# Kernel tuning notes

Hardware: AMD Instinct MI355X
Metric: run time of the kernel (lower is better)

Reference implementation:

```python
import jax, jax.numpy as jnp
import numpy as np

B, BAG, H, C = 512, 32, 1024, 53
EPS = 1e-8  # torch F.cosine_similarity denominator clamp


def setup_inputs() -> dict:
    key = jax.random.key(0)
    ks = jax.random.split(key, 5)
    return {
        "sent_reps": jax.random.normal(ks[0], (B, BAG, H), jnp.float32),
        "aug_sent_reps": jax.random.normal(ks[1], (B, BAG, H), jnp.float32),
        "rel_table": jax.random.normal(ks[2], (C, H), jnp.float32),
        "cls_w": jax.random.normal(ks[3], (C, H), jnp.float32) * 0.02,
        "cls_b": jnp.zeros((C,), jnp.float32),
        "labels": jax.random.randint(ks[4], (B,), 0, C),
        "temperature": jnp.asarray(0.1, jnp.float32),
    }


def _cl(rep, aug, bag_rep, T):
    # rep, aug: (B, bag, H); bag_rep: (B, H)
    nr = jnp.linalg.norm(rep, axis=-1)        # (B, bag)
    na = jnp.linalg.norm(aug, axis=-1)        # (B, bag)
    nb = jnp.linalg.norm(bag_rep, axis=-1)    # (B,)
    pos_sim = jnp.sum(rep * aug, axis=-1) / jnp.maximum(nr * na, EPS)  # (B, bag)
    pos = jnp.exp(pos_sim / T)
    # pair[c, j, b] = cos(rep[b, j], bag_rep[c])  -- matches torch permute/broadcast chain
    dots = jnp.einsum('bjh,ch->cjb', rep, bag_rep)               # (B, bag, B)
    denom = jnp.maximum(nb[:, None, None] * nr.T[None], EPS)      # (B, bag, B)
    pair = dots / denom
    idx = jnp.arange(rep.shape[0])
    axis_sim = pair[idx, :, idx]                                  # (B, bag): cos(rep[b,j], bag_rep[b])
    neg = jnp.exp(pair / T).sum(axis=2) - jnp.exp(axis_sim / T)   # (B, bag)
    return jnp.mean(-jnp.log(pos / (pos + neg)))


def reference(sent_reps, aug_sent_reps, rel_table, cls_w, cls_b, labels, temperature):
    # Selective attention per bag (scope slices are uniform bags of size BAG -> vectorized)
    rel = rel_table[labels]                                        # (B, H)
    scale = jnp.sqrt(jnp.asarray(H, sent_reps.dtype))
    scores = jnp.einsum('bh,bjh->bj', rel, sent_reps) / scale      # (B, bag)
    alphas = jax.nn.softmax(scores, axis=-1)
    bag_reps = jnp.einsum('bj,bjh->bh', alphas, sent_reps)         # (B, H)
    bag_out = bag_reps @ cls_w.T + cls_b                           # (B, C)  (dropout in eval = identity)
    cl_loss = _cl(sent_reps, aug_sent_reps, bag_reps, temperature)
    return bag_out, cl_loss
```

## Files before the change

### kernel.cpp

```cpp
#include <hip/hip_runtime.h>
#include <hip/hip_bf16.h>


typedef __bf16 bf16x8 __attribute__((ext_vector_type(8)));
typedef __bf16 bf16x4 __attribute__((ext_vector_type(4)));
typedef __bf16 bf16x2 __attribute__((ext_vector_type(2)));
typedef float  f32x4  __attribute__((ext_vector_type(4)));

__device__ inline float wsum(float v) {
    #pragma unroll
    for (int off = 32; off > 0; off >>= 1) v += __shfl_xor(v, off, 64);
    return v;
}

__device__ inline void gll16(const void* g, void* l) {
    __builtin_amdgcn_global_load_lds((const __attribute__((address_space(1))) void*)g,
                                     (__attribute__((address_space(3))) void*)l, 16, 0, 0);
}

__device__ inline f32x4 ntld(const float* p) {
    return __builtin_nontemporal_load((const f32x4*)p);
}

__global__ __launch_bounds__(512, 4) void kab(
    const float* __restrict__ sent, const float* __restrict__ aug,
    const float* __restrict__ rel_table, const int* __restrict__ labels,
    __bf16* __restrict__ repb, float* __restrict__ nr, float* __restrict__ pos_sim,
    const float* __restrict__ clsw, __bf16* __restrict__ cwb,
    __bf16* __restrict__ bagb, float* __restrict__ nbsq, float* __restrict__ loss)
{
    __shared__ __align__(16) __bf16 repS[32][1024];
    __shared__ float scoreS[32], alphaS[32], redS[8];
    const int b = blockIdx.x, t = threadIdx.x;
    const int w = t >> 6, lane = t & 63;

    if (b < 128) {
        const int i = b * 512 + t;
        cwb[i] = (i < 53 * 1024) ? (__bf16)clsw[i] : (__bf16)0.0f;
        if (b == 0 && t == 0) *loss = 0.0f;
    }

    const float* relp = rel_table + (size_t)labels[b] * 1024;
    #pragma unroll
    for (int rr = 0; rr < 4; rr++) {
        const int j = w * 4 + rr;
        const size_t rbase = ((size_t)b * 32 + j) * 1024;
        const float* srow = sent + rbase;
        const float* arow = aug + rbase;
        float P = 0.f, R = 0.f, A = 0.f, D = 0.f;
        #pragma unroll
        for (int i = 0; i < 4; i++) {
            const int h = i * 256 + lane * 4;
            f32x4 v  = ntld(srow + h);
            f32x4 a  = ntld(arow + h);
            f32x4 rl = *(const f32x4*)(relp + h);
            P += v.x * rl.x + v.y * rl.y + v.z * rl.z + v.w * rl.w;
            R += v.x * v.x + v.y * v.y + v.z * v.z + v.w * v.w;
            A += a.x * a.x + a.y * a.y + a.z * a.z + a.w * a.w;
            D += v.x * a.x + v.y * a.y + v.z * a.z + v.w * a.w;
            bf16x4 vb = { (__bf16)v.x, (__bf16)v.y, (__bf16)v.z, (__bf16)v.w };
            *(bf16x4*)(&repS[j][h]) = vb;
            *(bf16x4*)(repb + rbase + h) = vb;
        }
        #pragma unroll
        for (int off = 32; off > 0; off >>= 1) {
            P += __shfl_xor(P, off, 64);
            R += __shfl_xor(R, off, 64);
            A += __shfl_xor(A, off, 64);
            D += __shfl_xor(D, off, 64);
        }
        if (lane == 0) {
            scoreS[j] = P * (1.0f / 32.0f);
            float nrv = sqrtf(R), nav = sqrtf(A);
            nr[b * 32 + j] = nrv;
            pos_sim[b * 32 + j] = D / fmaxf(nrv * nav, 1e-8f);
        }
    }
    __syncthreads();

    if (t < 32) {
        float sj = scoreS[t], mx = sj;
        #pragma unroll
        for (int off = 16; off > 0; off >>= 1) mx = fmaxf(mx, __shfl_xor(mx, off, 32));
        float e = __expf(sj - mx), sm = e;
        #pragma unroll
        for (int off = 16; off > 0; off >>= 1) sm += __shfl_xor(sm, off, 32);
        alphaS[t] = e / sm;
    }
    __syncthreads();

    float b0 = 0.f, b1 = 0.f;
    #pragma unroll 8
    for (int j = 0; j < 32; j++) {
        const float al = alphaS[j];
        bf16x2 v = *(const bf16x2*)(&repS[j][t * 2]);
        b0 += al * (float)v.x;
        b1 += al * (float)v.y;
    }
    bf16x2 bb = { (__bf16)b0, (__bf16)b1 };
    *(bf16x2*)(bagb + (size_t)b * 1024 + t * 2) = bb;

    float q = b0 * b0 + b1 * b1;
    q = wsum(q);
    if (lane == 0) redS[w] = q;
    __syncthreads();
    if (t == 0)
        nbsq[b] = redS[0] + redS[1] + redS[2] + redS[3]
                + redS[4] + redS[5] + redS[6] + redS[7];
}

__global__ __launch_bounds__(256, 3) void k4_gemm(
    const __bf16* __restrict__ repb, const __bf16* __restrict__ bagb,
    const float* __restrict__ nr, const float* __restrict__ nbsq,
    const float* __restrict__ temp, float* __restrict__ partial, float* __restrict__ diag,
    const __bf16* __restrict__ cwb, const float* __restrict__ bias, float* __restrict__ out)
{
    __shared__ __align__(16) char smem[49152];
    const int bid = blockIdx.x;
    const int t = threadIdx.x, lane = t & 63, w = t >> 6;
    const int m = lane & 15, quad = lane >> 4;

    if (bid < 8) {
        __bf16* Al = (__bf16*)smem;
        __bf16* Bl = (__bf16*)(smem + 8192);
        const int r0 = bid * 64;
        f32x4 acc[4] = {};
        const int i0 = t * 8;
        const int row0 = i0 >> 5, kk0 = i0 & 31;
        const __bf16* gA = bagb + (size_t)(r0 + row0) * 1024 + kk0;
        const __bf16* gB = cwb + (size_t)row0 * 1024 + kk0;
        for (int k0 = 0; k0 < 1024; k0 += 64) {
            __syncthreads();
            gll16(gA + k0,      Al + i0);
            gll16(gA + k0 + 32, Al + 2048 + i0);
            gll16(gB + k0,      Bl + i0);
            gll16(gB + k0 + 32, Bl + 2048 + i0);
            __syncthreads();
            #pragma unroll
            for (int ks = 0; ks < 2; ks++) {
                bf16x8 a = *(const bf16x8*)(&Al[ks * 2048 + (w * 16 + m) * 32 + quad * 8]);
                #pragma unroll
                for (int n = 0; n < 4; n++) {
                    bf16x8 bf = *(const bf16x8*)(&Bl[ks * 2048 + (n * 16 + m) * 32 + quad * 8]);
                    acc[n] = __builtin_amdgcn_mfma_f32_16x16x32_bf16(a, bf, acc[n], 0, 0, 0);
                }
            }
        }
        #pragma unroll
        for (int n = 0; n < 4; n++) {
            const int c = n * 16 + m;
            if (c < 53) {
                #pragma unroll
                for (int i = 0; i < 4; i++) {
                    const int r = r0 + w * 16 + quad * 4 + i;
                    out[(size_t)r * 53 + c] = acc[n][i] + bias[c];
                }
            }
        }
        return;
    }

    float* negp2 = (float*)smem;

    const int gbid = bid - 8;
    const int xcd = gbid & 7, slot = gbid >> 3;
    const int cb = slot & 3, rb = (slot >> 2) * 8 + xcd;
    const int r0 = rb * 128, c0 = cb * 128;
    const int wr0 = (w & 1) * 64, wc0 = (w >> 1) * 64;

    const int srow = t >> 2;
    const int scol = 8 * ((t & 3) ^ ((srow >> 1) & 3));
    const __bf16* gA0 = repb + (size_t)(r0 + srow) * 1024 + scol;
    const __bf16* gA1 = gA0 + (size_t)64 * 1024;
    const __bf16* gB0 = bagb + (size_t)(c0 + srow) * 1024 + scol;
    const __bf16* gB1 = gB0 + (size_t)64 * 1024;
    const int dA0 = t * 8, dA1 = (t + 256) * 8;
    const int dB0 = 4096 + t * 8, dB1 = 4096 + (t + 256) * 8;

    const int rho = (m >> 1) & 3;
    const int offA = ((wr0 + m) * 4 + (quad ^ rho)) * 8;
    const int offB = 4096 + ((wc0 + m) * 4 + (quad ^ rho)) * 8;

    f32x4 acc[4][4] = {};

    #define BUFB(s) ((__bf16*)(smem + (((s) % 3) * 16384)))
    #define STG(s) do { const int kk_ = (s) * 32; __bf16* b_ = BUFB(s);     \
        gll16(gA0 + kk_, b_ + dA0); gll16(gA1 + kk_, b_ + dA1);             \
        gll16(gB0 + kk_, b_ + dB0); gll16(gB1 + kk_, b_ + dB1); } while (0)

    #define CMP(s) do { const __bf16* b_ = BUFB(s); bf16x8 av_[4], bv_[4];  \
        _Pragma("unroll") for (int i_ = 0; i_ < 4; i_++)                    \
            av_[i_] = *(const bf16x8*)(b_ + offA + i_ * 512);               \
        _Pragma("unroll") for (int n_ = 0; n_ < 4; n_++)                    \
            bv_[n_] = *(const bf16x8*)(b_ + offB + n_ * 512);               \
        _Pragma("unroll") for (int i_ = 0; i_ < 4; i_++)                    \
        _Pragma("unroll") for (int n_ = 0; n_ < 4; n_++)                    \
            acc[i_][n_] = __builtin_amdgcn_mfma_f32_16x16x32_bf16(          \
                av_[i_], bv_[n_], acc[i_][n_], 0, 0, 0); } while (0)

    #define FENCE(N) do { __builtin_amdgcn_sched_barrier(0);                \
        asm volatile("s_waitcnt vmcnt(" #N ")" ::: "memory");               \
        __builtin_amdgcn_s_barrier();                                       \
        __builtin_amdgcn_sched_barrier(0); } while (0)

    STG(0); STG(1);
    FENCE(4);
    #pragma unroll 1
    for (int s = 0; s < 30; ++s) {
        STG(s + 2);
        CMP(s);
        FENCE(4);
    }
    CMP(30); FENCE(0);
    CMP(31);
    __syncthreads();

    const float invT = 1.0f / *temp;
    float nrv[16];
    #pragma unroll
    for (int i = 0; i < 4; i++)
        #pragma unroll
        for (int g = 0; g < 4; g++)
            nrv[i * 4 + g] = nr[r0 + wr0 + i * 16 + quad * 4 + g];

    float* myneg = negp2 + (size_t)(w & 1) * 32 * 128;
    #pragma unroll
    for (int n = 0; n < 4; n++) {
        const int c_local = wc0 + n * 16 + m;
        const int cg = c0 + c_local;
        const float nbv = sqrtf(nbsq[cg]);
        #pragma unroll
        for (int i = 0; i < 2; i++) {
            #pragma unroll
            for (int g = 0; g < 4; g++) {
                const int jj = i * 16 + quad * 4 + g;
                const int rg0 = r0 + wr0 + i * 16 + quad * 4 + g;
                const int rg2 = rg0 + 32;
                float e0 = __expf(acc[i][n][g]     / fmaxf(nbv * nrv[i * 4 + g],       1e-8f) * invT);
                float e2 = __expf(acc[i + 2][n][g] / fmaxf(nbv * nrv[(i + 2) * 4 + g], 1e-8f) * invT);
                myneg[jj * 128 + c_local] = e0 + e2;
                if ((rg0 >> 5) == cg) diag[(size_t)cg * 32 + jj] = e0;
                if ((rg2 >> 5) == cg) diag[(size_t)cg * 32 + jj] = e2;
            }
        }
    }
    __syncthreads();

    float* pout = partial + (size_t)rb * 32 * 512 + c0;
    {
        const int jj = t >> 3, c16 = (t & 7) * 16;
        #pragma unroll
        for (int v = 0; v < 4; v++) {
            f32x4 a = *(const f32x4*)(negp2 + jj * 128 + c16 + v * 4);
            f32x4 bq = *(const f32x4*)(negp2 + 32 * 128 + jj * 128 + c16 + v * 4);
            *(f32x4*)(pout + (size_t)jj * 512 + c16 + v * 4) = a + bq;
        }
    }
    #undef BUFB
    #undef STG
    #undef CMP
    #undef FENCE
}

__global__ __launch_bounds__(256) void k5_neg(
    const float* __restrict__ partial, const float* __restrict__ diag,
    const float* __restrict__ pos_sim, const float* __restrict__ temp,
    float* __restrict__ loss)
{
    const int ct = blockIdx.x & 7, j = blockIdx.x >> 3;
    const int t = threadIdx.x, lane = t & 63, w = t >> 6;
    const int bsub = t >> 4;
    const int cidx = t & 15;
    f32x4 acc = {};
    #pragma unroll 4
    for (int r = 0; r < 8; r++) {
        const int rb = bsub * 8 + r;
        f32x4 v = *(const f32x4*)(partial + ((size_t)rb * 32 + j) * 512 + ct * 64 + cidx * 4);
        acc += v;
    }
    #pragma unroll
    for (int k = 0; k < 4; k++) {
        acc[k] += __shfl_xor(acc[k], 16, 64);
        acc[k] += __shfl_xor(acc[k], 32, 64);
    }
    __shared__ float red[4][64];
    if (lane < 16) {
        #pragma unroll
        for (int k = 0; k < 4; k++) red[w][lane * 4 + k] = acc[k];
    }
    __syncthreads();

    if (t < 64) {
        const int c = ct * 64 + t;
        float S = red[0][t] + red[1][t] + red[2][t] + red[3][t];
        S -= diag[(size_t)c * 32 + j];
        const float invT = 1.0f / *temp;
        const float lp = pos_sim[(c << 5) + j] * invT;
        float term = logf(__expf(lp) + S) - lp;
        term = wsum(term);
        if (t == 0) atomicAdd(loss, term * (1.0f / 16384.0f));
    }
}

extern "C" void kernel_launch(void* const* d_in, const int* in_sizes, int n_in,
                              void* d_out, int out_size, void* d_ws, size_t ws_size,
                              hipStream_t stream)
{
    const float* sent = (const float*)d_in[0];
    const float* aug  = (const float*)d_in[1];
    const float* rel  = (const float*)d_in[2];
    const float* clsw = (const float*)d_in[3];
    const float* clsb = (const float*)d_in[4];
    const int*   lab  = (const int*)d_in[5];
    const float* temp = (const float*)d_in[6];
    float* out = (float*)d_out;

    char* ws = (char*)d_ws;
    __bf16* bagb    = (__bf16*)(ws);
    float*  nbsq    = (float*)(ws + (1u << 20));
    float*  nr      = (float*)(ws + (1u << 20) + 64 * 1024);
    float*  pos     = (float*)(ws + (1u << 20) + 128 * 1024);
    __bf16* cwb     = (__bf16*)(ws + (1u << 20) + 192 * 1024);
    float*  diag    = (float*)(ws + (2u << 20) + 64 * 1024);
    __bf16* repb    = (__bf16*)(ws + (4u << 20));
    float*  partial = (float*)(ws + (36u << 20));

    float* loss = out + 27136;

    kab    <<<512, 512, 0, stream>>>(sent, aug, rel, lab, repb, nr, pos,
                                     clsw, cwb, bagb, nbsq, loss);
    k4_gemm<<<520, 256, 0, stream>>>(repb, bagb, nr, nbsq, temp, partial, diag,
                                     cwb, clsb, out);
    k5_neg <<<256, 256, 0, stream>>>(partial, diag, pos, temp, loss);
}
```

Before: 189.8 us.

## Load B operand directly from global into registers, shrinking LDS staging

The bag-rep (B) operand of the contrastive GEMM tile is now loaded straight from global memory into registers with double-buffered register sets, and only the rep (A) operand is staged through LDS. This halves LDS use per block, which could allow more blocks per CU, and removes the LDS read traffic for B. The cost is more vector registers and uncoalesced 16-byte per-lane global loads whose latency must be hidden by the vmcnt fences, which are retuned to match.

```diff
diff --git a/kernel.cpp b/kernel.cpp
--- a/kernel.cpp
+++ b/kernel.cpp
@@ -115,7 +115,7 @@
     const float* __restrict__ temp, float* __restrict__ partial, float* __restrict__ diag,
     const __bf16* __restrict__ cwb, const float* __restrict__ bias, float* __restrict__ out)
 {
-    __shared__ __align__(16) char smem[49152];
+    __shared__ __align__(16) char smem[32768];
     const int bid = blockIdx.x;
     const int t = threadIdx.x, lane = t & 63, w = t >> 6;
     const int m = lane & 15, quad = lane >> 4;
@@ -172,31 +172,34 @@
     const int scol = 8 * ((t & 3) ^ ((srow >> 1) & 3));
     const __bf16* gA0 = repb + (size_t)(r0 + srow) * 1024 + scol;
     const __bf16* gA1 = gA0 + (size_t)64 * 1024;
-    const __bf16* gB0 = bagb + (size_t)(c0 + srow) * 1024 + scol;
-    const __bf16* gB1 = gB0 + (size_t)64 * 1024;
     const int dA0 = t * 8, dA1 = (t + 256) * 8;
-    const int dB0 = 4096 + t * 8, dB1 = 4096 + (t + 256) * 8;
 
     const int rho = (m >> 1) & 3;
     const int offA = ((wr0 + m) * 4 + (quad ^ rho)) * 8;
-    const int offB = 4096 + ((wc0 + m) * 4 + (quad ^ rho)) * 8;
+
+    const __bf16* pB[4];
+    #pragma unroll
+    for (int n = 0; n < 4; n++)
+        pB[n] = bagb + (size_t)(c0 + wc0 + n * 16 + m) * 1024 + quad * 8;
 
     f32x4 acc[4][4] = {};
-
-    #define BUFB(s) ((__bf16*)(smem + (((s) % 3) * 16384)))
+    bf16x8 bvA[4], bvB[4];
+
+    #define BUFB(s) ((__bf16*)(smem + (((s) % 3) * 8192)))
     #define STG(s) do { const int kk_ = (s) * 32; __bf16* b_ = BUFB(s);     \
-        gll16(gA0 + kk_, b_ + dA0); gll16(gA1 + kk_, b_ + dA1);             \
-        gll16(gB0 + kk_, b_ + dB0); gll16(gB1 + kk_, b_ + dB1); } while (0)
-
-    #define CMP(s) do { const __bf16* b_ = BUFB(s); bf16x8 av_[4], bv_[4];  \
+        gll16(gA0 + kk_, b_ + dA0); gll16(gA1 + kk_, b_ + dA1); } while (0)
+
+    #define LDB(dst, s) do { const int kk_ = (s) * 32;                      \
+        _Pragma("unroll") for (int n_ = 0; n_ < 4; n_++)                    \
+            dst[n_] = *(const bf16x8*)(pB[n_] + kk_); } while (0)
+
+    #define CMP(s, bv) do { const __bf16* b_ = BUFB(s); bf16x8 av_[4];      \
         _Pragma("unroll") for (int i_ = 0; i_ < 4; i_++)                    \
             av_[i_] = *(const bf16x8*)(b_ + offA + i_ * 512);               \
-        _Pragma("unroll") for (int n_ = 0; n_ < 4; n_++)                    \
-            bv_[n_] = *(const bf16x8*)(b_ + offB + n_ * 512);               \
         _Pragma("unroll") for (int i_ = 0; i_ < 4; i_++)                    \
         _Pragma("unroll") for (int n_ = 0; n_ < 4; n_++)                    \
             acc[i_][n_] = __builtin_amdgcn_mfma_f32_16x16x32_bf16(          \
-                av_[i_], bv_[n_], acc[i_][n_], 0, 0, 0); } while (0)
+                av_[i_], bv[n_], acc[i_][n_], 0, 0, 0); } while (0)
 
     #define FENCE(N) do { __builtin_amdgcn_sched_barrier(0);                \
         asm volatile("s_waitcnt vmcnt(" #N ")" ::: "memory");               \
@@ -204,15 +207,20 @@
         __builtin_amdgcn_sched_barrier(0); } while (0)
 
     STG(0); STG(1);
-    FENCE(4);
+    LDB(bvA, 0);
     #pragma unroll 1
-    for (int s = 0; s < 30; ++s) {
-        STG(s + 2);
-        CMP(s);
-        FENCE(4);
-    }
-    CMP(30); FENCE(0);
-    CMP(31);
+    for (int s = 0; s < 28; s += 2) {
+        LDB(bvB, s + 1); STG(s + 2);
+        FENCE(6);
+        CMP(s, bvA);
+        LDB(bvA, s + 2); STG(s + 3);
+        FENCE(6);
+        CMP(s + 1, bvB);
+    }
+    LDB(bvB, 29); STG(30); FENCE(6); CMP(28, bvA);
+    LDB(bvA, 30); STG(31); FENCE(6); CMP(29, bvB);
+    LDB(bvB, 31);          FENCE(4); CMP(30, bvA);
+    FENCE(0);                        CMP(31, bvB);
     __syncthreads();
 
     const float invT = 1.0f / *temp;
@@ -258,6 +266,7 @@
     }
     #undef BUFB
     #undef STG
+    #undef LDB
     #undef CMP
     #undef FENCE
 }
```

Measured after the change: 205.9 us. 1.08x slower.
